# Kernel optimization log

Measured on AMD Instinct MI355X. Metric: run time of the kernel, lower is better.

## Reference

```python
import jax, jax.numpy as jnp
import numpy as np

B, Q, K, D, H = 8, 200, 16384, 256, 8
ALIGN_K, CROSS_K, FF = 96, 1024, 1024
DH = D // H

def _l2norm(x):
    n = jnp.linalg.norm(x, axis=-1, keepdims=True)
    return x / jnp.maximum(n, 1e-6)

def _layernorm(x, g, b):
    mu = jnp.mean(x, axis=-1, keepdims=True)
    v = jnp.var(x, axis=-1, keepdims=True)
    return (x - mu) / jnp.sqrt(v + 1e-5) * g + b

def _mha(xq, xk, xv, in_w, in_b, out_w, out_b, bias=None):
    # torch nn.MultiheadAttention (batch_first, eval mode)
    wq, wk, wv = jnp.split(in_w, 3, axis=0)
    bq, bk, bv = jnp.split(in_b, 3, axis=0)
    def heads(x, w, bb):
        y = x @ w.T + bb
        return y.reshape(x.shape[0], x.shape[1], H, DH).transpose(0, 2, 1, 3)
    qh, kh, vh = heads(xq, wq, bq), heads(xk, wk, bk), heads(xv, wv, bv)
    s = jnp.einsum('bhqd,bhkd->bhqk', qh, kh) / (DH ** 0.5)
    if bias is not None:
        s = s + bias
    a = jax.nn.softmax(s, axis=-1)
    o = jnp.einsum('bhqk,bhkd->bhqd', a, vh).transpose(0, 2, 1, 3).reshape(xq.shape[0], xq.shape[1], D)
    return o @ out_w.T + out_b

def setup_inputs():
    key = jax.random.key(0)
    ks = jax.random.split(key, 40)
    r = lambda i, sh, s=1.0: jax.random.normal(ks[i], sh, jnp.float32) * s
    W = 0.02
    return dict(
        q=r(0, (B, Q, D)), q_pos=r(1, (B, Q, D)), memory=r(2, (B, K, D)),
        cross_attn_bias=r(3, (B, Q, K), 0.1),
        align_wq=r(4, (D, D), W), align_wm=r(5, (D, D), W),
        gate_w1=r(6, (D, 2 * D), W), gate_b1=jnp.zeros((D,), jnp.float32),
        gate_w2=r(7, (D, D), W), gate_b2=jnp.zeros((D,), jnp.float32),
        cross_wq=r(8, (D, D), W), cross_wm=r(9, (D, D), W),
        sa_in_w=r(10, (3 * D, D), W), sa_in_b=jnp.zeros((3 * D,), jnp.float32),
        sa_out_w=r(11, (D, D), W), sa_out_b=jnp.zeros((D,), jnp.float32),
        ca_in_w=r(12, (3 * D, D), W), ca_in_b=jnp.zeros((3 * D,), jnp.float32),
        ca_out_w=r(13, (D, D), W), ca_out_b=jnp.zeros((D,), jnp.float32),
        ffn_w1=r(14, (FF, D), W), ffn_b1=jnp.zeros((FF,), jnp.float32),
        ffn_w2=r(15, (D, FF), W), ffn_b2=jnp.zeros((D,), jnp.float32),
        n1_g=jnp.ones((D,), jnp.float32), n1_b=jnp.zeros((D,), jnp.float32),
        n2_g=jnp.ones((D,), jnp.float32), n2_b=jnp.zeros((D,), jnp.float32),
        n3_g=jnp.ones((D,), jnp.float32), n3_b=jnp.zeros((D,), jnp.float32))

def reference(q, q_pos, memory, cross_attn_bias, align_wq, align_wm, gate_w1, gate_b1,
              gate_w2, gate_b2, cross_wq, cross_wm, sa_in_w, sa_in_b, sa_out_w, sa_out_b,
              ca_in_w, ca_in_b, ca_out_w, ca_out_b, ffn_w1, ffn_b1, ffn_w2, ffn_b2,
              n1_g, n1_b, n2_g, n2_b, n3_g, n3_b):
    # --- query-memory align: proj+normalize+sim+topk+gather+softmax+weighted-sum ---
    qn = _l2norm(q @ align_wq.T)
    mn = _l2norm(memory @ align_wm.T)
    sim = jnp.einsum('bqd,bkd->bqk', qn, mn)            # [B,Q,K]
    vals, idx = jax.lax.top_k(sim, ALIGN_K)             # [B,Q,ALIGN_K]
    selected = jax.vmap(lambda m, i: m[i])(memory, idx) # [B,Q,ALIGN_K,D]
    w = jax.nn.softmax(vals, axis=-1)
    aligned = jnp.einsum('bqk,bqkd->bqd', w, selected)
    h = jax.nn.gelu(jnp.concatenate([q, aligned], axis=-1) @ gate_w1.T + gate_b1, approximate=False)
    gate = jax.nn.sigmoid(h @ gate_w2.T + gate_b2)
    qx = q + gate * aligned
    # --- self attention ---
    qk = qx + q_pos
    q2 = _mha(qk, qk, qx, sa_in_w, sa_in_b, sa_out_w, sa_out_b)
    qx = _layernorm(qx + q2, n1_g, n1_b)
    # --- cross-memory sparsify (topk over K) ---
    qn2 = _l2norm(qx @ cross_wq.T)
    mn2 = _l2norm(memory @ cross_wm.T)
    sim2 = jnp.einsum('bqd,bkd->bqk', qn2, mn2)
    importance = sim2.max(axis=1)                       # [B,K]
    _, kidx = jax.lax.top_k(importance, CROSS_K)        # [B,CROSS_K]
    mem_sel = jax.vmap(lambda m, i: m[i])(memory, kidx) # [B,CROSS_K,D]
    bias_sel = jnp.take_along_axis(
        cross_attn_bias, jnp.broadcast_to(kidx[:, None, :], (B, Q, CROSS_K)), axis=2)
    bias4 = jnp.broadcast_to(bias_sel[:, None], (B, H, Q, CROSS_K))
    q2 = _mha(qx + q_pos, mem_sel, mem_sel, ca_in_w, ca_in_b, ca_out_w, ca_out_b, bias4)
    qx = _layernorm(qx + q2, n2_g, n2_b)
    # --- FFN ---
    f = jax.nn.gelu(qx @ ffn_w1.T + ffn_b1, approximate=False) @ ffn_w2.T + ffn_b2
    return _layernorm(qx + f, n3_g, n3_b)
```

## Files before the change

kernel.cpp:

```cpp
#include <hip/hip_runtime.h>
#include <hip/hip_bf16.h>
#include <math.h>

#define B_ 8
#define Q_ 200
#define K_ 16384
#define D_ 256
#define H_ 8
#define DH_ 32
#define ALIGNK_ 96
#define CROSSK_ 1024
#define FF_ 1024
#define BQ_ (B_*Q_)
#define BK_ (B_*K_)

typedef unsigned short u16;
typedef short bf16x8 __attribute__((ext_vector_type(8)));
typedef float f32x4 __attribute__((ext_vector_type(4)));

__device__ __forceinline__ float b2f(u16 u){ return __uint_as_float(((unsigned)u)<<16); }
__device__ __forceinline__ u16 f2b(float f){
  unsigned x = __float_as_uint(f);
  unsigned r = x + 0x7FFFu + ((x>>16)&1u);
  return (u16)(r>>16);
}
__device__ __forceinline__ unsigned p2u(float lo, float hi){
  return (unsigned)f2b(lo) | ((unsigned)f2b(hi)<<16);
}
__device__ __forceinline__ uint4 pk8(float4 a, float4 b){
  return make_uint4(p2u(a.x,a.y), p2u(a.z,a.w), p2u(b.x,b.y), p2u(b.z,b.w));
}
__device__ __forceinline__ unsigned fkey(float f){ unsigned b=__float_as_uint(f); return (b&0x80000000u)? ~b : (b|0x80000000u); }
__device__ __forceinline__ float funkey(unsigned k){ unsigned b=(k&0x80000000u)? (k^0x80000000u) : ~k; return __uint_as_float(b); }
__device__ __forceinline__ float gelu_f(float x){ return 0.5f*x*(1.0f+erff(x*0.70710678118654752f)); }
__device__ __forceinline__ float sigmoid_f(float x){ return 1.0f/(1.0f+__expf(-x)); }

struct GArgs {
  const void* A; const void* B; const float* bias;
  float* Cf; u16* Cb; unsigned* amax;
  const int* gather;
  long lda, ldb, ldc;
  long sA, sB, sC, sAmax, sGather;
  int M, N, K, act;
};

template<int AF32, int BF32>
__global__ __launch_bounds__(256) void gemm_bt(GArgs g)
{
  const int tid = threadIdx.x;
  const int bz = blockIdx.z;
  const int m0 = blockIdx.y*64, n0 = blockIdx.x*64;
  const int lane = tid & 63, wave = tid >> 6;
  const int wr = wave >> 1, wc = wave & 1;
  __shared__ __align__(16) u16 As[64][72];
  __shared__ __align__(16) u16 Bs[64][72];
  f32x4 acc[2][2] = {};

  const int lrow = tid>>2;
  const int lk = (tid&3)*16;
  int ar = m0 + lrow; if (ar > g.M-1) ar = g.M-1;
  if (g.gather) ar = g.gather[(long)bz*g.sGather + ar];
  int br = n0 + lrow; if (br > g.N-1) br = g.N-1;
  long aoff = (long)bz*g.sA + (long)ar*g.lda + lk;
  long boff = (long)bz*g.sB + (long)br*g.ldb + lk;

  const int nk = g.K >> 6;
  for (int kt=0; kt<nk; ++kt){
    uint4 wa0, wa1, wb0, wb1;
    if (AF32){
      const float* p = (const float*)g.A + aoff;
      float4 f0 = *(const float4*)(p+0);
      float4 f1 = *(const float4*)(p+4);
      float4 f2v= *(const float4*)(p+8);
      float4 f3 = *(const float4*)(p+12);
      wa0 = pk8(f0,f1); wa1 = pk8(f2v,f3);
    } else {
      const u16* p = (const u16*)g.A + aoff;
      wa0 = *(const uint4*)p; wa1 = *(const uint4*)(p+8);
    }
    if (BF32){
      const float* p = (const float*)g.B + boff;
      float4 f0 = *(const float4*)(p+0);
      float4 f1 = *(const float4*)(p+4);
      float4 f2v= *(const float4*)(p+8);
      float4 f3 = *(const float4*)(p+12);
      wb0 = pk8(f0,f1); wb1 = pk8(f2v,f3);
    } else {
      const u16* p = (const u16*)g.B + boff;
      wb0 = *(const uint4*)p; wb1 = *(const uint4*)(p+8);
    }
    aoff += 64; boff += 64;
    __syncthreads();
    *(uint4*)&As[lrow][lk]   = wa0; *(uint4*)&As[lrow][lk+8] = wa1;
    *(uint4*)&Bs[lrow][lk]   = wb0; *(uint4*)&Bs[lrow][lk+8] = wb1;
    __syncthreads();
    #pragma unroll
    for (int kk=0; kk<2; ++kk){
      const int ko = kk*32 + (lane>>4)*8;
      bf16x8 af0 = *(const bf16x8*)&As[wr*32      + (lane&15)][ko];
      bf16x8 af1 = *(const bf16x8*)&As[wr*32 + 16 + (lane&15)][ko];
      bf16x8 bf0 = *(const bf16x8*)&Bs[wc*32      + (lane&15)][ko];
      bf16x8 bf1 = *(const bf16x8*)&Bs[wc*32 + 16 + (lane&15)][ko];
      acc[0][0] = __builtin_amdgcn_mfma_f32_16x16x32_bf16(af0, bf0, acc[0][0], 0,0,0);
      acc[0][1] = __builtin_amdgcn_mfma_f32_16x16x32_bf16(af0, bf1, acc[0][1], 0,0,0);
      acc[1][0] = __builtin_amdgcn_mfma_f32_16x16x32_bf16(af1, bf0, acc[1][0], 0,0,0);
      acc[1][1] = __builtin_amdgcn_mfma_f32_16x16x32_bf16(af1, bf1, acc[1][1], 0,0,0);
    }
  }

  if (g.amax){
    #pragma unroll
    for (int j=0;j<2;j++){
      float mx = -3.0e38f;
      #pragma unroll
      for (int i=0;i<2;i++)
        #pragma unroll
        for (int r=0;r<4;r++) mx = fmaxf(mx, acc[i][j][r]);
      mx = fmaxf(mx, __shfl_xor(mx, 16));
      mx = fmaxf(mx, __shfl_xor(mx, 32));
      if ((lane>>4)==0){
        int n = n0 + wc*32 + j*16 + (lane&15);
        if (n < g.N) atomicMax(&g.amax[(long)bz*g.sAmax + n], fkey(mx));
      }
    }
    return;
  }

  #pragma unroll
  for (int i=0;i<2;i++)
  #pragma unroll
  for (int j=0;j<2;j++)
  #pragma unroll
  for (int r=0;r<4;r++){
    int m = m0 + wr*32 + i*16 + (lane>>4)*4 + r;
    int n = n0 + wc*32 + j*16 + (lane&15);
    if (m < g.M && n < g.N){
      float v = acc[i][j][r];
      if (g.bias) v += g.bias[n];
      if (g.act==1) v = gelu_f(v);
      else if (g.act==2) v = sigmoid_f(v);
      long ci = (long)bz*g.sC + (long)m*g.ldc + n;
      if (g.Cf) g.Cf[ci] = v; else g.Cb[ci] = f2b(v);
    }
  }
}

__global__ void w2b_kernel(const float* w, u16* wb, int n)
{
  int i = (blockIdx.x*256 + threadIdx.x)*8;
  if (i < n){
    float4 a = *(const float4*)(w+i), b = *(const float4*)(w+i+4);
    *(uint4*)(wb+i) = pk8(a,b);
  }
}

template<int AF32>
__global__ __launch_bounds__(256) void proj_l2norm(
    const void* Ain, long lda, const u16* Wb, u16* outp, int R)
{
  __shared__ __align__(16) u16 As[64][72];
  __shared__ __align__(16) u16 Bs[64][72];
  const int tid = threadIdx.x;
  const int m0 = blockIdx.x*64;
  const int lane = tid & 63, wave = tid >> 6;
  f32x4 acc[4][4] = {};

  const int lrow = tid>>2, lk = (tid&3)*16;
  int ar = m0 + lrow; if (ar > R-1) ar = R-1;

  for (int kt=0; kt<4; ++kt){
    uint4 wa0, wa1;
    if (AF32){
      const float* p = (const float*)Ain + (long)ar*lda + kt*64 + lk;
      wa0 = pk8(*(const float4*)(p+0), *(const float4*)(p+4));
      wa1 = pk8(*(const float4*)(p+8), *(const float4*)(p+12));
    } else {
      const u16* p = (const u16*)Ain + (long)ar*lda + kt*64 + lk;
      wa0 = *(const uint4*)p; wa1 = *(const uint4*)(p+8);
    }
    #pragma unroll
    for (int nc=0; nc<4; ++nc){
      const u16* wp = Wb + (long)(nc*64 + lrow)*256 + kt*64 + lk;
      uint4 wb0 = *(const uint4*)wp;
      uint4 wb1 = *(const uint4*)(wp+8);
      __syncthreads();
      if (nc==0){ *(uint4*)&As[lrow][lk] = wa0; *(uint4*)&As[lrow][lk+8] = wa1; }
      *(uint4*)&Bs[lrow][lk] = wb0; *(uint4*)&Bs[lrow][lk+8] = wb1;
      __syncthreads();
      #pragma unroll
      for (int kk=0; kk<2; ++kk){
        const int ko = kk*32 + (lane>>4)*8;
        bf16x8 af = *(const bf16x8*)&As[wave*16 + (lane&15)][ko];
        #pragma unroll
        for (int j=0; j<4; j++){
          bf16x8 bfr = *(const bf16x8*)&Bs[j*16 + (lane&15)][ko];
          acc[nc][j] = __builtin_amdgcn_mfma_f32_16x16x32_bf16(af, bfr, acc[nc][j], 0,0,0);
        }
      }
    }
  }

  #pragma unroll
  for (int r=0;r<4;r++){
    float ssq = 0.f;
    #pragma unroll
    for (int nc=0;nc<4;nc++)
      #pragma unroll
      for (int j=0;j<4;j++) ssq += acc[nc][j][r]*acc[nc][j][r];
    ssq += __shfl_xor(ssq,1); ssq += __shfl_xor(ssq,2);
    ssq += __shfl_xor(ssq,4); ssq += __shfl_xor(ssq,8);
    float inv = 1.0f/fmaxf(sqrtf(ssq), 1e-6f);
    int row = m0 + wave*16 + (lane>>4)*4 + r;
    if (row < R){
      u16* op = outp + (long)row*256 + (lane&15);
      #pragma unroll
      for (int nc=0;nc<4;nc++)
        #pragma unroll
        for (int j=0;j<4;j++) op[nc*64 + j*16] = f2b(acc[nc][j][r]*inv);
    }
  }
}

__global__ __launch_bounds__(256) void topk_kernel(const float* inF, const unsigned* inK,
    long in_stride, int RANK, float* out_val, int* out_idx)
{
  __shared__ int red[2][4];
  __shared__ int redt[4];
  __shared__ int poss;
  int row = blockIdx.x, tid = threadIdx.x;
  unsigned kr[64];
  if (inF){
    const float4* p = (const float4*)(inF + (long)row*in_stride);
    #pragma unroll
    for (int jj=0;jj<16;jj++){
      float4 v = p[tid + jj*256];
      kr[jj*4+0]=fkey(v.x); kr[jj*4+1]=fkey(v.y); kr[jj*4+2]=fkey(v.z); kr[jj*4+3]=fkey(v.w);
    }
  } else {
    const uint4* p = (const uint4*)(inK + (long)row*in_stride);
    #pragma unroll
    for (int jj=0;jj<16;jj++){
      uint4 v = p[tid + jj*256];
      kr[jj*4+0]=v.x; kr[jj*4+1]=v.y; kr[jj*4+2]=v.z; kr[jj*4+3]=v.w;
    }
  }
  if (tid==0) poss = 0;

  unsigned u = 0; bool exact = false; int pp = 0;
  for (int bit=31; bit>=0; --bit){
    unsigned cand = u | (1u<<bit);
    int c = 0;
    #pragma unroll
    for (int j=0;j<64;j++) c += (kr[j] >= cand) ? 1 : 0;
    #pragma unroll
    for (int off=32; off; off>>=1) c += __shfl_down(c, off);
    if ((tid&63)==0) red[pp][tid>>6] = c;
    __syncthreads();
    c = red[pp][0]+red[pp][1]+red[pp][2]+red[pp][3];
    pp ^= 1;
    if (c >= RANK){
      u = cand;
      if (c == RANK){ exact = true; break; }
    }
  }

  int t = 0;
  if (!exact){
    int cgt = 0;
    #pragma unroll
    for (int j=0;j<64;j++) cgt += (kr[j] > u) ? 1 : 0;
    #pragma unroll
    for (int off=32; off; off>>=1) cgt += __shfl_down(cgt, off);
    __syncthreads();
    if ((tid&63)==0) redt[tid>>6] = cgt;
    __syncthreads();
    cgt = redt[0]+redt[1]+redt[2]+redt[3];
    int Req = RANK - cgt;
    for (int bit=13; bit>=0; --bit){
      int cand = t | (1<<bit);
      int c = 0;
      #pragma unroll
      for (int j=0;j<64;j++){
        int e = (tid<<2) + (j&3) + ((j>>2)<<10);
        c += (kr[j]==u && e < cand) ? 1 : 0;
      }
      #pragma unroll
      for (int off=32; off; off>>=1) c += __shfl_down(c, off);
      __syncthreads();
      if ((tid&63)==0) redt[tid>>6] = c;
      __syncthreads();
      c = redt[0]+redt[1]+redt[2]+redt[3];
      if (c < Req) t = cand;
    }
  }
  __syncthreads();
  #pragma unroll
  for (int j=0;j<64;j++){
    int e = (tid<<2) + (j&3) + ((j>>2)<<10);
    unsigned kk = kr[j];
    bool win = exact ? (kk >= u) : (kk > u || (kk == u && e <= t));
    if (win){
      int p2 = atomicAdd(&poss, 1);
      out_val[(long)row*RANK + p2] = funkey(kk);
      out_idx[(long)row*RANK + p2] = e;
    }
  }
}

__global__ __launch_bounds__(256) void align_combine(const float* vals, const int* idx,
    const float* memory, float* alignedv)
{
  __shared__ float w[96];
  __shared__ int id[96];
  __shared__ float reds[2];
  int row = blockIdx.x, tid = threadIdx.x;
  int b = row / 200;
  if (tid < 96){ w[tid] = vals[(long)row*96 + tid]; id[tid] = idx[(long)row*96 + tid]; }
  __syncthreads();
  if (tid < 64){
    float a = w[tid];
    float bb2 = (tid < 32) ? w[64+tid] : -3e38f;
    float m = fmaxf(a, bb2);
    #pragma unroll
    for (int off=32; off; off>>=1) m = fmaxf(m, __shfl_xor(m, off));
    if (tid==0) reds[0] = m;
  }
  __syncthreads();
  float m = reds[0];
  if (tid < 96) w[tid] = __expf(w[tid]-m);
  __syncthreads();
  if (tid < 64){
    float a = w[tid] + ((tid<32)? w[64+tid] : 0.f);
    #pragma unroll
    for (int off=32; off; off>>=1) a += __shfl_xor(a, off);
    if (tid==0) reds[1] = a;
  }
  __syncthreads();
  float invs = 1.0f/reds[1];
  float acc = 0.f;
  const float* mb = memory + (long)b*K_*D_;
  for (int k=0;k<96;k++) acc += w[k] * mb[(long)id[k]*D_ + tid];
  alignedv[(long)row*256 + tid] = acc*invs;
}

__global__ void make_cat(const float* q, const float* alignedv, u16* cat)
{
  int row = blockIdx.x, tid = threadIdx.x;
  long i = (long)row*256 + tid;
  cat[(long)row*512 + tid]       = f2b(q[i]);
  cat[(long)row*512 + 256 + tid] = f2b(alignedv[i]);
}

__global__ void combine_gate(const float* q, const float* q_pos, const float* alignedv,
    const float* gate, float* qx, u16* qx_b, u16* qk_b)
{
  int row = blockIdx.x, tid = threadIdx.x;
  long i = (long)row*256 + tid;
  float v = q[i] + gate[i]*alignedv[i];
  qx[i] = v;
  qx_b[i] = f2b(v);
  qk_b[i] = f2b(v + q_pos[i]);
}

__global__ __launch_bounds__(256) void add_ln(const float* x, const float* y,
    const float* g, const float* bb, const float* q_pos,
    float* out_f, u16* out_b, u16* out_pos_b)
{
  __shared__ float red[8];
  int row = blockIdx.x, tid = threadIdx.x;
  long i = (long)row*256 + tid;
  float t = fminf(fmaxf(x[i] + y[i], -1e6f), 1e6f);
  float s1 = t, s2 = t*t;
  #pragma unroll
  for (int off=32; off; off>>=1){ s1 += __shfl_down(s1,off); s2 += __shfl_down(s2,off); }
  if ((tid&63)==0){ red[(tid>>6)*2] = s1; red[(tid>>6)*2+1] = s2; }
  __syncthreads();
  s1 = red[0]+red[2]+red[4]+red[6];
  s2 = red[1]+red[3]+red[5]+red[7];
  float mu = s1 * (1.0f/256.0f);
  float var = fmaxf(s2 * (1.0f/256.0f) - mu*mu, 0.f);
  float rstd = rsqrtf(var + 1e-5f);
  float v = (t-mu)*rstd*g[tid] + bb[tid];
  if (out_f) out_f[i] = v;
  if (out_b) out_b[i] = f2b(v);
  if (out_pos_b) out_pos_b[i] = f2b(v + q_pos[i]);
}

__global__ void fill_u32(unsigned* p, unsigned val, int n)
{ int i = blockIdx.x*256 + threadIdx.x; if (i<n) p[i] = val; }

__global__ __launch_bounds__(256) void bias_gather(const float* cbias, const int* kidx,
    float* biasT)
{
  int b = blockIdx.y;
  int j = blockIdx.x*8 + (threadIdx.x>>5);
  int q = threadIdx.x & 31;
  int kid = kidx[b*CROSSK_ + j];
  const float* src = cbias + (long)b*Q_*K_ + kid;
  float* dst = biasT + ((long)b*CROSSK_ + j)*200;
  for (int qq=q; qq<200; qq+=32) dst[qq] = src[(long)qq*K_];
}

__global__ __launch_bounds__(256) void attn_kernel(
    const u16* Qb, int q_stride,
    const u16* KVb, int kv_stride, int k_off, int v_off, int Lk,
    const float* biasT,
    int nsplit, int chunk,
    float* opart, float* mlpart, float scale)
{
  __shared__ float Ks[64][36];
  __shared__ float Vs[64][36];
  const int b = blockIdx.z, h = blockIdx.y;
  const int split = blockIdx.x % nsplit;
  const int q0 = (blockIdx.x / nsplit) * 64;
  const int tid = threadIdx.x;
  const int cg = tid & 3, r = tid >> 2;
  const int kbeg = split*chunk;
  int kend = kbeg + chunk; if (kend > Lk) kend = Lk;

  int qr = q0 + r; if (qr > 199) qr = 199;
  float qreg[32];
  {
    const u16* qp = Qb + (long)(b*200+qr)*q_stride + h*32;
    #pragma unroll
    for (int w=0; w<4; w++){
      uint4 u = *(const uint4*)(qp + w*8);
      qreg[w*8+0]=b2f((u16)(u.x&0xffffu))*scale; qreg[w*8+1]=b2f((u16)(u.x>>16))*scale;
      qreg[w*8+2]=b2f((u16)(u.y&0xffffu))*scale; qreg[w*8+3]=b2f((u16)(u.y>>16))*scale;
      qreg[w*8+4]=b2f((u16)(u.z&0xffffu))*scale; qreg[w*8+5]=b2f((u16)(u.z>>16))*scale;
      qreg[w*8+6]=b2f((u16)(u.w&0xffffu))*scale; qreg[w*8+7]=b2f((u16)(u.w>>16))*scale;
    }
  }
  const float* bT = biasT ? biasT + ((long)b*CROSSK_)*200 + qr : nullptr;

  float o32[32];
  #pragma unroll
  for (int i=0;i<32;i++) o32[i]=0.f;
  float mrun = -3e38f, lrun = 0.f;

  const int srow = tid>>2, sc8 = (tid&3)*8;
  for (int j0=kbeg; j0<kend; j0+=64){
    int kr = j0 + srow; if (kr > kend-1) kr = kend-1;
    const long base = (long)(b*Lk + kr)*kv_stride;
    uint4 ku = *(const uint4*)(KVb + base + k_off + sc8);
    uint4 vu = *(const uint4*)(KVb + base + v_off + sc8);
    __syncthreads();
    {
      float4 f0, f1;
      f0.x=b2f((u16)(ku.x&0xffffu)); f0.y=b2f((u16)(ku.x>>16)); f0.z=b2f((u16)(ku.y&0xffffu)); f0.w=b2f((u16)(ku.y>>16));
      f1.x=b2f((u16)(ku.z&0xffffu)); f1.y=b2f((u16)(ku.z>>16)); f1.z=b2f((u16)(ku.w&0xffffu)); f1.w=b2f((u16)(ku.w>>16));
      *(float4*)&Ks[srow][sc8] = f0; *(float4*)&Ks[srow][sc8+4] = f1;
      f0.x=b2f((u16)(vu.x&0xffffu)); f0.y=b2f((u16)(vu.x>>16)); f0.z=b2f((u16)(vu.y&0xffffu)); f0.w=b2f((u16)(vu.y>>16));
      f1.x=b2f((u16)(vu.z&0xffffu)); f1.y=b2f((u16)(vu.z>>16)); f1.z=b2f((u16)(vu.w&0xffffu)); f1.w=b2f((u16)(vu.w>>16));
      *(float4*)&Vs[srow][sc8] = f0; *(float4*)&Vs[srow][sc8+4] = f1;
    }
    __syncthreads();

    float sv[16];
    float mloc = -3e38f;
    #pragma unroll
    for (int jj=0;jj<16;jj++){
      const int c = cg + jj*4;
      const float4* kp = (const float4*)&Ks[c][0];
      float a = 0.f;
      #pragma unroll
      for (int dq=0;dq<8;dq++){
        float4 kv = kp[dq];
        a += qreg[dq*4+0]*kv.x + qreg[dq*4+1]*kv.y + qreg[dq*4+2]*kv.z + qreg[dq*4+3]*kv.w;
      }
      if (biasT) a += bT[(long)(j0 + c)*200];
      if (j0 + c >= kend) a = -3e38f;
      sv[jj] = a; mloc = fmaxf(mloc, a);
    }
    mloc = fmaxf(mloc, __shfl_xor(mloc,1));
    mloc = fmaxf(mloc, __shfl_xor(mloc,2));
    const float mnew = fmaxf(mrun, mloc);
    const float alpha = __expf(mrun - mnew);
    float lloc = 0.f;
    #pragma unroll
    for (int jj=0;jj<16;jj++){
      float p = (j0 + cg + jj*4 >= kend) ? 0.f : __expf(sv[jj]-mnew);
      sv[jj] = p; lloc += p;
    }
    lloc += __shfl_xor(lloc,1);
    lloc += __shfl_xor(lloc,2);
    lrun = lrun*alpha + lloc;
    #pragma unroll
    for (int i=0;i<32;i++) o32[i] *= alpha;
    #pragma unroll
    for (int jj=0;jj<16;jj++){
      const int c = cg + jj*4;
      const float p = sv[jj];
      const float4* vp = (const float4*)&Vs[c][0];
      #pragma unroll
      for (int dq=0;dq<8;dq++){
        float4 v = vp[dq];
        o32[dq*4+0] += p*v.x; o32[dq*4+1] += p*v.y; o32[dq*4+2] += p*v.z; o32[dq*4+3] += p*v.w;
      }
    }
    mrun = mnew;
  }

  #pragma unroll
  for (int d=0;d<32;d++){
    float v = o32[d];
    v += __shfl_xor(v,1);
    v += __shfl_xor(v,2);
    o32[d] = v;
  }
  if (q0 + r < 200){
    const long pbase = (((long)(b*H_+h)*nsplit + split)*200) + (q0 + r);
    float* op = opart + pbase*32;
    #pragma unroll
    for (int i=0;i<8;i++) op[cg*8+i] = o32[cg*8+i];
    if (cg==0){ mlpart[pbase*2] = mrun; mlpart[pbase*2+1] = lrun; }
  }
}

__global__ __launch_bounds__(256) void attn_combine(const float* opart, const float* mlpart,
    int nsplit, u16* outp)
{
  int row = blockIdx.x;
  int b = row/200, qi = row%200;
  int tid = threadIdx.x;
  int h = tid>>5, d = tid&31;
  const long base = ((long)(b*H_+h)*nsplit)*200 + qi;
  float M = -3e38f;
  for (int s=0;s<nsplit;s++) M = fmaxf(M, mlpart[(base + (long)s*200)*2]);
  float L = 0.f, acc = 0.f;
  for (int s=0;s<nsplit;s++){
    const long ix = base + (long)s*200;
    float w = __expf(mlpart[ix*2] - M);
    L   += mlpart[ix*2+1]*w;
    acc += opart[ix*32 + d]*w;
  }
  outp[(long)row*256 + h*32 + d] = f2b(acc / fmaxf(L, 1e-30f));
}

extern "C" void kernel_launch(void* const* d_in, const int* in_sizes, int n_in,
                              void* d_out, int out_size, void* d_ws, size_t ws_size,
                              hipStream_t stream)
{
  const float* q        = (const float*)d_in[0];
  const float* q_pos    = (const float*)d_in[1];
  const float* memory   = (const float*)d_in[2];
  const float* cbias    = (const float*)d_in[3];
  const float* align_wq = (const float*)d_in[4];
  const float* align_wm = (const float*)d_in[5];
  const float* gate_w1  = (const float*)d_in[6];
  const float* gate_b1  = (const float*)d_in[7];
  const float* gate_w2  = (const float*)d_in[8];
  const float* gate_b2  = (const float*)d_in[9];
  const float* cross_wq = (const float*)d_in[10];
  const float* cross_wm = (const float*)d_in[11];
  const float* sa_in_w  = (const float*)d_in[12];
  const float* sa_in_b  = (const float*)d_in[13];
  const float* sa_out_w = (const float*)d_in[14];
  const float* sa_out_b = (const float*)d_in[15];
  const float* ca_in_w  = (const float*)d_in[16];
  const float* ca_in_b  = (const float*)d_in[17];
  const float* ca_out_w = (const float*)d_in[18];
  const float* ca_out_b = (const float*)d_in[19];
  const float* ffn_w1   = (const float*)d_in[20];
  const float* ffn_b1   = (const float*)d_in[21];
  const float* ffn_w2   = (const float*)d_in[22];
  const float* ffn_b2   = (const float*)d_in[23];
  const float* n1_g = (const float*)d_in[24];
  const float* n1_b = (const float*)d_in[25];
  const float* n2_g = (const float*)d_in[26];
  const float* n2_b = (const float*)d_in[27];
  const float* n3_g = (const float*)d_in[28];
  const float* n3_b = (const float*)d_in[29];
  float* out = (float*)d_out;

  char* wsb = (char*)d_ws;
  size_t off = 0;
  auto alloc = [&](size_t bytes)->char*{
    char* p = wsb + off; off = (off + bytes + 255) & ~(size_t)255; return p;
  };
  const int NSPLIT = 4;
  u16*    qn_bf   = (u16*)   alloc((size_t)BQ_*D_*2);
  float*  vals96  = (float*) alloc((size_t)BQ_*96*4);
  int*    idx96   = (int*)   alloc((size_t)BQ_*96*4);
  float*  alignedv= (float*) alloc((size_t)BQ_*D_*4);
  u16*    cat_bf  = (u16*)   alloc((size_t)BQ_*512*2);
  u16*    h_bf    = (u16*)   alloc((size_t)BQ_*D_*2);
  float*  gatebuf = (float*) alloc((size_t)BQ_*D_*4);
  float*  qx      = (float*) alloc((size_t)BQ_*D_*4);
  u16*    qx_bf   = (u16*)   alloc((size_t)BQ_*D_*2);
  u16*    qk_bf   = (u16*)   alloc((size_t)BQ_*D_*2);
  u16*    qpos2_bf= (u16*)   alloc((size_t)BQ_*D_*2);
  u16*    qkv_bf  = (u16*)   alloc((size_t)BQ_*768*2);
  u16*    attO_bf = (u16*)   alloc((size_t)BQ_*D_*2);
  float*  q2      = (float*) alloc((size_t)BQ_*D_*4);
  unsigned* imp   = (unsigned*)alloc((size_t)B_*K_*4);
  int*    kidx    = (int*)   alloc((size_t)B_*CROSSK_*4);
  u16*    cq_bf   = (u16*)   alloc((size_t)BQ_*D_*2);
  u16*    f1_bf   = (u16*)   alloc((size_t)BQ_*FF_*2);
  float*  f2buf   = (float*) alloc((size_t)BQ_*D_*4);
  float*  opart   = (float*) alloc((size_t)B_*H_*NSPLIT*200*32*4);
  float*  mlpart  = (float*) alloc((size_t)B_*H_*NSPLIT*200*2*4);
  float*  biasT   = (float*) alloc((size_t)B_*CROSSK_*200*4);
  u16*    wb_alwq = (u16*)   alloc((size_t)D_*D_*2);
  u16*    wb_alwm = (u16*)   alloc((size_t)D_*D_*2);
  u16*    wb_crwq = (u16*)   alloc((size_t)D_*D_*2);
  u16*    wb_crwm = (u16*)   alloc((size_t)D_*D_*2);

  const size_t kv_bytes   = (size_t)B_*CROSSK_*512*2;
  const size_t mn_full    = (size_t)BK_*D_*2;
  const size_t mn_small   = (size_t)K_*D_*2;
  const size_t sim_full   = (size_t)BQ_*K_*4;
  size_t remain = (ws_size > off) ? ws_size - off : 0;
  bool fullws = remain >= mn_full + sim_full + (1u<<20);
  size_t mn_bytes = fullws ? mn_full : (mn_small > kv_bytes ? mn_small : kv_bytes);
  int simRows;
  if (fullws) simRows = BQ_;
  else {
    size_t left = (remain > mn_bytes + (1u<<18)) ? remain - mn_bytes - (1u<<18) : 0;
    long r = (long)(left / ((size_t)K_*4));
    simRows = (int)(r < 8 ? 8 : (r > Q_ ? Q_ : r));
  }
  u16*   mn_bf  = (u16*)  alloc(mn_bytes);
  u16*   kvbuf  = (u16*)  mn_bf;
  float* simbuf = (float*)alloc((size_t)simRows*K_*4);

  auto gemm = [&](int af32, int bf32,
                  const void* A, long lda, long sA,
                  const void* Bm, long ldb, long sB,
                  int M, int N, int Kd,
                  const float* bias, int act,
                  float* Cf, u16* Cb, long ldc, long sC,
                  unsigned* amax, long sAmax,
                  const int* gather, long sGather, int Z){
    GArgs ga;
    ga.A=A; ga.B=Bm; ga.bias=bias; ga.Cf=Cf; ga.Cb=Cb; ga.amax=amax; ga.gather=gather;
    ga.lda=lda; ga.ldb=ldb; ga.ldc=ldc; ga.sA=sA; ga.sB=sB; ga.sC=sC;
    ga.sAmax=sAmax; ga.sGather=sGather;
    ga.M=M; ga.N=N; ga.K=Kd; ga.act=act;
    dim3 grid(N/64, (M+63)/64, Z);
    if (af32 && bf32)      gemm_bt<1,1><<<grid, 256, 0, stream>>>(ga);
    else if (af32)         gemm_bt<1,0><<<grid, 256, 0, stream>>>(ga);
    else if (bf32)         gemm_bt<0,1><<<grid, 256, 0, stream>>>(ga);
    else                   gemm_bt<0,0><<<grid, 256, 0, stream>>>(ga);
  };
  const float ascale = 0.17677669529663687f;

  w2b_kernel<<<32,256,0,stream>>>(align_wq, wb_alwq, D_*D_);
  w2b_kernel<<<32,256,0,stream>>>(align_wm, wb_alwm, D_*D_);
  w2b_kernel<<<32,256,0,stream>>>(cross_wq, wb_crwq, D_*D_);
  w2b_kernel<<<32,256,0,stream>>>(cross_wm, wb_crwm, D_*D_);

  proj_l2norm<1><<<BQ_/64,256,0,stream>>>(q, 256, wb_alwq, qn_bf, BQ_);
  if (fullws){
    proj_l2norm<1><<<BK_/64,256,0,stream>>>(memory, 256, wb_alwm, mn_bf, BK_);
    gemm(0,0, qn_bf,256,(long)200*256, mn_bf,256,(long)K_*256, 200,K_,256,
         nullptr,0, simbuf,nullptr,K_,(long)200*K_, nullptr,0, nullptr,0, B_);
    topk_kernel<<<BQ_,256,0,stream>>>(simbuf, nullptr, K_, 96, vals96, idx96);
  } else {
    for (int b=0;b<B_;b++){
      proj_l2norm<1><<<K_/64,256,0,stream>>>(memory + (size_t)b*K_*256, 256, wb_alwm, mn_bf, K_);
      for (int q0=0; q0<Q_; q0+=simRows){
        int rows = (Q_ - q0 < simRows) ? (Q_ - q0) : simRows;
        gemm(0,0, qn_bf + ((size_t)b*200+q0)*256,256,0, mn_bf,256,0, rows,K_,256,
             nullptr,0, simbuf,nullptr,K_,0, nullptr,0, nullptr,0, 1);
        topk_kernel<<<rows,256,0,stream>>>(simbuf, nullptr, K_, 96,
             vals96 + ((size_t)b*200+q0)*96, idx96 + ((size_t)b*200+q0)*96);
      }
    }
  }
  align_combine<<<BQ_,256,0,stream>>>(vals96, idx96, memory, alignedv);

  make_cat<<<BQ_,256,0,stream>>>(q, alignedv, cat_bf);
  gemm(0,1, cat_bf,512,0, gate_w1,512,0, BQ_,256,512, gate_b1,1, nullptr,h_bf,256,0, nullptr,0, nullptr,0, 1);
  gemm(0,1, h_bf,256,0, gate_w2,256,0, BQ_,256,256, gate_b2,2, gatebuf,nullptr,256,0, nullptr,0, nullptr,0, 1);
  combine_gate<<<BQ_,256,0,stream>>>(q, q_pos, alignedv, gatebuf, qx, qx_bf, qk_bf);

  gemm(0,1, qk_bf,256,0, sa_in_w,256,0, BQ_,512,256, sa_in_b,0, nullptr,qkv_bf,768,0, nullptr,0, nullptr,0, 1);
  gemm(0,1, qx_bf,256,0, sa_in_w+512*256,256,0, BQ_,256,256, sa_in_b+512,0, nullptr,qkv_bf+512,768,0, nullptr,0, nullptr,0, 1);
  attn_kernel<<<dim3(4*NSPLIT,H_,B_),256,0,stream>>>(qkv_bf,768, qkv_bf,768,256,512,200,
      nullptr, NSPLIT,64, opart,mlpart, ascale);
  attn_combine<<<BQ_,256,0,stream>>>(opart, mlpart, NSPLIT, attO_bf);
  gemm(0,1, attO_bf,256,0, sa_out_w,256,0, BQ_,256,256, sa_out_b,0, q2,nullptr,256,0, nullptr,0, nullptr,0, 1);
  add_ln<<<BQ_,256,0,stream>>>(qx, q2, n1_g, n1_b, q_pos, qx, qx_bf, qpos2_bf);

  proj_l2norm<0><<<BQ_/64,256,0,stream>>>(qx_bf, 256, wb_crwq, qn_bf, BQ_);
  fill_u32<<<(B_*K_+255)/256,256,0,stream>>>(imp, 0u, B_*K_);
  if (fullws){
    proj_l2norm<1><<<BK_/64,256,0,stream>>>(memory, 256, wb_crwm, mn_bf, BK_);
    gemm(0,0, qn_bf,256,(long)200*256, mn_bf,256,(long)K_*256, 200,K_,256,
         nullptr,0, nullptr,nullptr,0,0, imp,(long)K_, nullptr,0, B_);
  } else {
    for (int b=0;b<B_;b++){
      proj_l2norm<1><<<K_/64,256,0,stream>>>(memory + (size_t)b*K_*256, 256, wb_crwm, mn_bf, K_);
      gemm(0,0, qn_bf + (size_t)b*200*256,256,0, mn_bf,256,0, 200,K_,256,
           nullptr,0, nullptr,nullptr,0,0, imp + (size_t)b*K_,(long)K_, nullptr,0, 1);
    }
  }
  topk_kernel<<<B_,256,0,stream>>>(nullptr, imp, K_, CROSSK_, vals96 , kidx);

  bias_gather<<<dim3(CROSSK_/8, B_),256,0,stream>>>(cbias, kidx, biasT);
  gemm(1,1, memory,256,(long)K_*256, ca_in_w+256*256,256,0, CROSSK_,512,256,
       ca_in_b+256,0, nullptr,kvbuf,512,(long)CROSSK_*512, nullptr,0, kidx,(long)CROSSK_, B_);
  gemm(0,1, qpos2_bf,256,0, ca_in_w,256,0, BQ_,256,256, ca_in_b,0, nullptr,cq_bf,256,0, nullptr,0, nullptr,0, 1);
  attn_kernel<<<dim3(4*NSPLIT,H_,B_),256,0,stream>>>(cq_bf,256, kvbuf,512,0,256,CROSSK_,
      biasT, NSPLIT,256, opart,mlpart, ascale);
  attn_combine<<<BQ_,256,0,stream>>>(opart, mlpart, NSPLIT, attO_bf);
  gemm(0,1, attO_bf,256,0, ca_out_w,256,0, BQ_,256,256, ca_out_b,0, q2,nullptr,256,0, nullptr,0, nullptr,0, 1);
  add_ln<<<BQ_,256,0,stream>>>(qx, q2, n2_g, n2_b, nullptr, qx, qx_bf, nullptr);

  gemm(0,1, qx_bf,256,0, ffn_w1,256,0, BQ_,FF_,256, ffn_b1,1, nullptr,f1_bf,FF_,0, nullptr,0, nullptr,0, 1);
  gemm(0,1, f1_bf,FF_,0, ffn_w2,FF_,0, BQ_,256,FF_, ffn_b2,0, f2buf,nullptr,256,0, nullptr,0, nullptr,0, 1);
  add_ln<<<BQ_,256,0,stream>>>(qx, f2buf, n3_g, n3_b, nullptr, out, nullptr, nullptr);

  (void)in_sizes; (void)n_in; (void)out_size;
}
```

Baseline: 916.0 us.

## Replace fused scalar attention with MFMA score, softmax, and PV kernels

When the full workspace is available, the fp32 flash-style attention kernel (plus its split-combine pass) is replaced by three kernels: an MFMA bf16 QK^T score kernel, a row softmax that writes bf16 probabilities, and an MFMA P·V kernel. The cross-attention bias gather is changed to a query-major layout, so each thread reads contiguous kidx entries instead of strided rows across K. The scalar FMA work moves onto matrix cores, at the price of materialising the full score and probability matrices in global memory and adding extra launches. Probabilities are rounded to bf16 before PV, which slightly lowers precision.

```diff
diff --git a/kernel.cpp b/kernel.cpp
--- a/kernel.cpp
+++ b/kernel.cpp
@@ -389,22 +389,135 @@
 __global__ void fill_u32(unsigned* p, unsigned val, int n)
 { int i = blockIdx.x*256 + threadIdx.x; if (i<n) p[i] = val; }
 
-__global__ __launch_bounds__(256) void bias_gather(const float* cbias, const int* kidx,
-    float* biasT)
-{
-  int b = blockIdx.y;
-  int j = blockIdx.x*8 + (threadIdx.x>>5);
-  int q = threadIdx.x & 31;
-  int kid = kidx[b*CROSSK_ + j];
-  const float* src = cbias + (long)b*Q_*K_ + kid;
-  float* dst = biasT + ((long)b*CROSSK_ + j)*200;
-  for (int qq=q; qq<200; qq+=32) dst[qq] = src[(long)qq*K_];
+__global__ __launch_bounds__(256) void bias_gather2(const float* cbias, const int* kidx,
+    float* biasTq)
+{
+  int qq = blockIdx.x, b = blockIdx.y;
+  const float* src = cbias + ((long)b*200+qq)*(long)K_;
+  float* dst = biasTq + ((long)b*200+qq)*CROSSK_;
+  const int* kp = kidx + b*CROSSK_;
+  for (int j=threadIdx.x; j<CROSSK_; j+=256) dst[j] = src[kp[j]];
+}
+
+__global__ __launch_bounds__(256) void qk_score(
+    const u16* Qb, int q_stride, const u16* KVb, int kv_stride, int k_off,
+    int Lk, int Jpad, const float* biasTq, float* S, float scale)
+{
+  __shared__ __align__(16) u16 Qs[64][40];
+  __shared__ __align__(16) u16 Ks[64][40];
+  const int bh = blockIdx.z, b = bh>>3, h = bh&7;
+  const int q0 = blockIdx.y*64, j0 = blockIdx.x*64;
+  const int tid = threadIdx.x, lane = tid&63, w = tid>>6;
+  {
+    int row = tid>>2, c8 = (tid&3)*8;
+    int qr = q0+row; if (qr>199) qr=199;
+    *(uint4*)&Qs[row][c8] = *(const uint4*)(Qb + (long)(b*200+qr)*q_stride + h*32 + c8);
+    int j = j0+row;
+    uint4 kv = make_uint4(0,0,0,0);
+    if (j < Lk) kv = *(const uint4*)(KVb + (long)(b*Lk+j)*kv_stride + k_off + c8);
+    *(uint4*)&Ks[row][c8] = kv;
+  }
+  __syncthreads();
+  bf16x8 af = *(const bf16x8*)&Qs[w*16 + (lane&15)][(lane>>4)*8];
+  f32x4 acc[4];
+  #pragma unroll
+  for (int jj=0;jj<4;jj++){
+    f32x4 zz = {};
+    bf16x8 bfr = *(const bf16x8*)&Ks[jj*16 + (lane&15)][(lane>>4)*8];
+    acc[jj] = __builtin_amdgcn_mfma_f32_16x16x32_bf16(af, bfr, zz, 0,0,0);
+  }
+  #pragma unroll
+  for (int jj=0;jj<4;jj++)
+  #pragma unroll
+  for (int r=0;r<4;r++){
+    int q = q0 + w*16 + (lane>>4)*4 + r;
+    int j = j0 + jj*16 + (lane&15);
+    if (q < 200){
+      float s = acc[jj][r]*scale;
+      if (biasTq) s += biasTq[((long)(b*200+q))*Jpad + j];
+      if (j >= Lk) s = -3e38f;
+      S[((long)bh*200 + q)*Jpad + j] = s;
+    }
+  }
+}
+
+template<int JP>
+__global__ __launch_bounds__(256) void softmax_p(const float* S, u16* P)
+{
+  __shared__ float red[8];
+  const long base = (long)blockIdx.x * JP;
+  const int tid = threadIdx.x;
+  constexpr int PER = JP/256;
+  float v[PER];
+  float m = -3e38f;
+  #pragma unroll
+  for (int i=0;i<PER;i++){ v[i] = S[base + tid + i*256]; m = fmaxf(m, v[i]); }
+  #pragma unroll
+  for (int off=32; off; off>>=1) m = fmaxf(m, __shfl_xor(m, off));
+  if ((tid&63)==0) red[tid>>6] = m;
+  __syncthreads();
+  m = fmaxf(fmaxf(red[0],red[1]), fmaxf(red[2],red[3]));
+  float s = 0.f;
+  #pragma unroll
+  for (int i=0;i<PER;i++){ v[i] = __expf(v[i]-m); s += v[i]; }
+  #pragma unroll
+  for (int off=32; off; off>>=1) s += __shfl_xor(s, off);
+  if ((tid&63)==0) red[4+(tid>>6)] = s;
+  __syncthreads();
+  s = red[4]+red[5]+red[6]+red[7];
+  float inv = 1.0f/s;
+  #pragma unroll
+  for (int i=0;i<PER;i++) P[base + tid + i*256] = f2b(v[i]*inv);
+}
+
+__global__ __launch_bounds__(256) void pv_kernel(
+    const u16* P, int Jpad, const u16* KVb, int kv_stride, int v_off, int Lk,
+    u16* outp)
+{
+  __shared__ __align__(16) u16 Vt[32][72];
+  const int bh = blockIdx.y, b = bh>>3, h = bh&7;
+  const int q0 = blockIdx.x*64;
+  const int tid = threadIdx.x, lane = tid&63, w = tid>>6;
+  f32x4 acc[2] = {};
+  int qa = q0 + w*16 + (lane&15); if (qa>199) qa=199;
+  const u16* Prow = P + ((long)bh*200 + qa)*Jpad;
+  const int jrow = lane;
+  const int d0 = w*8;
+
+  for (int j0=0; j0<Jpad; j0+=64){
+    int j = j0 + jrow;
+    uint4 vv = make_uint4(0,0,0,0);
+    if (j < Lk) vv = *(const uint4*)(KVb + (long)(b*Lk+j)*kv_stride + v_off + d0);
+    __syncthreads();
+    Vt[d0+0][jrow] = (u16)(vv.x&0xffffu); Vt[d0+1][jrow] = (u16)(vv.x>>16);
+    Vt[d0+2][jrow] = (u16)(vv.y&0xffffu); Vt[d0+3][jrow] = (u16)(vv.y>>16);
+    Vt[d0+4][jrow] = (u16)(vv.z&0xffffu); Vt[d0+5][jrow] = (u16)(vv.z>>16);
+    Vt[d0+6][jrow] = (u16)(vv.w&0xffffu); Vt[d0+7][jrow] = (u16)(vv.w>>16);
+    __syncthreads();
+    #pragma unroll
+    for (int ks=0; ks<2; ks++){
+      bf16x8 af = *(const bf16x8*)(Prow + j0 + ks*32 + (lane>>4)*8);
+      #pragma unroll
+      for (int dd=0; dd<2; dd++){
+        bf16x8 bfr = *(const bf16x8*)&Vt[dd*16 + (lane&15)][ks*32 + (lane>>4)*8];
+        acc[dd] = __builtin_amdgcn_mfma_f32_16x16x32_bf16(af, bfr, acc[dd], 0,0,0);
+      }
+    }
+  }
+  #pragma unroll
+  for (int dd=0; dd<2; dd++)
+  #pragma unroll
+  for (int r=0; r<4; r++){
+    int qq = q0 + w*16 + (lane>>4)*4 + r;
+    if (qq < 200)
+      outp[((long)(b*200+qq))*256 + h*32 + dd*16 + (lane&15)] = f2b(acc[dd][r]);
+  }
 }
 
 __global__ __launch_bounds__(256) void attn_kernel(
     const u16* Qb, int q_stride,
     const u16* KVb, int kv_stride, int k_off, int v_off, int Lk,
-    const float* biasT,
+    const float* biasTq,
     int nsplit, int chunk,
     float* opart, float* mlpart, float scale)
 {
@@ -431,7 +544,7 @@
       qreg[w*8+6]=b2f((u16)(u.w&0xffffu))*scale; qreg[w*8+7]=b2f((u16)(u.w>>16))*scale;
     }
   }
-  const float* bT = biasT ? biasT + ((long)b*CROSSK_)*200 + qr : nullptr;
+  const float* bT = biasTq ? biasTq + ((long)(b*200+qr))*CROSSK_ : nullptr;
 
   float o32[32];
   #pragma unroll
@@ -468,7 +581,7 @@
         float4 kv = kp[dq];
         a += qreg[dq*4+0]*kv.x + qreg[dq*4+1]*kv.y + qreg[dq*4+2]*kv.z + qreg[dq*4+3]*kv.w;
       }
-      if (biasT) a += bT[(long)(j0 + c)*200];
+      if (bT) a += bT[j0 + c];
       if (j0 + c >= kend) a = -3e38f;
       sv[jj] = a; mloc = fmaxf(mloc, a);
     }
@@ -600,7 +713,7 @@
   float*  f2buf   = (float*) alloc((size_t)BQ_*D_*4);
   float*  opart   = (float*) alloc((size_t)B_*H_*NSPLIT*200*32*4);
   float*  mlpart  = (float*) alloc((size_t)B_*H_*NSPLIT*200*2*4);
-  float*  biasT   = (float*) alloc((size_t)B_*CROSSK_*200*4);
+  float*  biasTq  = (float*) alloc((size_t)B_*Q_*CROSSK_*4);
   u16*    wb_alwq = (u16*)   alloc((size_t)D_*D_*2);
   u16*    wb_alwm = (u16*)   alloc((size_t)D_*D_*2);
   u16*    wb_crwq = (u16*)   alloc((size_t)D_*D_*2);
@@ -623,6 +736,8 @@
   u16*   mn_bf  = (u16*)  alloc(mn_bytes);
   u16*   kvbuf  = (u16*)  mn_bf;
   float* simbuf = (float*)alloc((size_t)simRows*K_*4);
+  float* Sbuf = simbuf;
+  u16*   Pbuf = (u16*)(simbuf + (size_t)64*200*1024);
 
   auto gemm = [&](int af32, int bf32,
                   const void* A, long lda, long sA,
@@ -677,9 +792,16 @@
 
   gemm(0,1, qk_bf,256,0, sa_in_w,256,0, BQ_,512,256, sa_in_b,0, nullptr,qkv_bf,768,0, nullptr,0, nullptr,0, 1);
   gemm(0,1, qx_bf,256,0, sa_in_w+512*256,256,0, BQ_,256,256, sa_in_b+512,0, nullptr,qkv_bf+512,768,0, nullptr,0, nullptr,0, 1);
-  attn_kernel<<<dim3(4*NSPLIT,H_,B_),256,0,stream>>>(qkv_bf,768, qkv_bf,768,256,512,200,
-      nullptr, NSPLIT,64, opart,mlpart, ascale);
-  attn_combine<<<BQ_,256,0,stream>>>(opart, mlpart, NSPLIT, attO_bf);
+  if (fullws){
+    qk_score<<<dim3(256/64, 4, B_*H_),256,0,stream>>>(qkv_bf,768, qkv_bf,768,256,
+        200, 256, nullptr, Sbuf, ascale);
+    softmax_p<256><<<B_*H_*200,256,0,stream>>>(Sbuf, Pbuf);
+    pv_kernel<<<dim3(4, B_*H_),256,0,stream>>>(Pbuf, 256, qkv_bf,768,512, 200, attO_bf);
+  } else {
+    attn_kernel<<<dim3(4*NSPLIT,H_,B_),256,0,stream>>>(qkv_bf,768, qkv_bf,768,256,512,200,
+        nullptr, NSPLIT,64, opart,mlpart, ascale);
+    attn_combine<<<BQ_,256,0,stream>>>(opart, mlpart, NSPLIT, attO_bf);
+  }
   gemm(0,1, attO_bf,256,0, sa_out_w,256,0, BQ_,256,256, sa_out_b,0, q2,nullptr,256,0, nullptr,0, nullptr,0, 1);
   add_ln<<<BQ_,256,0,stream>>>(qx, q2, n1_g, n1_b, q_pos, qx, qx_bf, qpos2_bf);
 
@@ -698,13 +820,20 @@
   }
   topk_kernel<<<B_,256,0,stream>>>(nullptr, imp, K_, CROSSK_, vals96 , kidx);
 
-  bias_gather<<<dim3(CROSSK_/8, B_),256,0,stream>>>(cbias, kidx, biasT);
+  bias_gather2<<<dim3(Q_, B_),256,0,stream>>>(cbias, kidx, biasTq);
   gemm(1,1, memory,256,(long)K_*256, ca_in_w+256*256,256,0, CROSSK_,512,256,
        ca_in_b+256,0, nullptr,kvbuf,512,(long)CROSSK_*512, nullptr,0, kidx,(long)CROSSK_, B_);
   gemm(0,1, qpos2_bf,256,0, ca_in_w,256,0, BQ_,256,256, ca_in_b,0, nullptr,cq_bf,256,0, nullptr,0, nullptr,0, 1);
-  attn_kernel<<<dim3(4*NSPLIT,H_,B_),256,0,stream>>>(cq_bf,256, kvbuf,512,0,256,CROSSK_,
-      biasT, NSPLIT,256, opart,mlpart, ascale);
-  attn_combine<<<BQ_,256,0,stream>>>(opart, mlpart, NSPLIT, attO_bf);
+  if (fullws){
+    qk_score<<<dim3(CROSSK_/64, 4, B_*H_),256,0,stream>>>(cq_bf,256, kvbuf,512,0,
+        CROSSK_, CROSSK_, biasTq, Sbuf, ascale);
+    softmax_p<1024><<<B_*H_*200,256,0,stream>>>(Sbuf, Pbuf);
+    pv_kernel<<<dim3(4, B_*H_),256,0,stream>>>(Pbuf, CROSSK_, kvbuf,512,256, CROSSK_, attO_bf);
+  } else {
+    attn_kernel<<<dim3(4*NSPLIT,H_,B_),256,0,stream>>>(cq_bf,256, kvbuf,512,0,256,CROSSK_,
+        biasTq, NSPLIT,256, opart,mlpart, ascale);
+    attn_combine<<<BQ_,256,0,stream>>>(opart, mlpart, NSPLIT, attO_bf);
+  }
   gemm(0,1, attO_bf,256,0, ca_out_w,256,0, BQ_,256,256, ca_out_b,0, q2,nullptr,256,0, nullptr,0, nullptr,0, 1);
   add_ln<<<BQ_,256,0,stream>>>(qx, q2, n2_g, n2_b, nullptr, qx, qx_bf, nullptr);
 
```

After: 938.5 us. +2.4%, slower.
